# Kernel optimization log

Measured on AMD Instinct MI355X. Metric: run time of the kernel, lower is better.

Reference implementation:

```python
import jax, jax.numpy as jnp
import numpy as np

N = 16384
MUL0, MUL1, MUL2 = 128, 64, 32            # multiplicities of 0e, 1e, 2e
A = 16                                    # node_attr_dim (Ax0e)
D0, D1, D2 = MUL0, MUL1 * 3, MUL2 * 5     # e3nn flat block sizes
DIN = D0 + D1 + D2                        # 480
NGATE = MUL1 + MUL2                       # 96 gate scalars
OUT0 = MUL0 + NGATE                       # 224 scalar (0e) outputs of fctp_1


def setup_inputs() -> dict:
    key = jax.random.key(0)
    ks = jax.random.split(key, 10)
    f32 = jnp.float32
    return {
        "node_vec": jax.random.normal(ks[0], (N, DIN), f32),
        "node_embedding": jax.random.normal(ks[1], (N, A), f32),
        # fctp_1 path weights (fully-connected TP with Ax0e attr)
        "W1_l0": jax.random.normal(ks[2], (MUL0, A, OUT0), f32),
        "W1_l1": jax.random.normal(ks[3], (MUL1, A, MUL1), f32),
        "W1_l2": jax.random.normal(ks[4], (MUL2, A, MUL2), f32),
        "b1": jnp.zeros((OUT0,), f32),
        # fctp_2 scalar-path weight (only 0e x 0e -> 0e path exists)
        "W2": jax.random.normal(ks[5], (MUL0, A, A), f32),
        "b2": jnp.zeros((A,), f32),
        # scalar readout MLP: LinearRS -> SiLU -> LinearRS
        "W3": jax.random.normal(ks[6], (A, A), f32),
        "b3": jnp.zeros((A,), f32),
        "W4": jax.random.normal(ks[7], (A, 1), f32),
        "b4": jnp.zeros((1,), f32),
    }


def reference(node_vec, node_embedding, W1_l0, W1_l1, W1_l2, b1, W2, b2, W3, b3, W4, b4):
    # split e3nn-layout features into per-l blocks [N, mul, 2l+1]
    x0 = node_vec[:, :D0]                               # [N, 128]   l=0
    x1 = node_vec[:, D0:D0 + D1].reshape(-1, MUL1, 3)   # [N, 64, 3] l=1
    x2 = node_vec[:, D0 + D1:].reshape(-1, MUL2, 5)     # [N, 32, 5] l=2
    a = node_embedding                                  # [N, A] 0e scalars
    # fctp_1: fully-connected TP with Ax0e attr -> per-l bilinear mix (path-normalized)
    s = jnp.einsum('ni,na,iak->nk', x0, a, W1_l0) / np.sqrt(MUL0 * A) + b1  # [N, 224]
    y1 = jnp.einsum('nim,na,iak->nkm', x1, a, W1_l1) / np.sqrt(MUL1 * A)    # [N, 64, 3]
    y2 = jnp.einsum('nim,na,iak->nkm', x2, a, W1_l2) / np.sqrt(MUL2 * A)    # [N, 32, 5]
    # SwishGate: SiLU on scalars, sigmoid gates multiply the l>0 channels
    scalars = jax.nn.silu(s[:, :MUL0])
    gates = jax.nn.sigmoid(s[:, MUL0:])
    y1 = y1 * gates[:, :MUL1, None]
    y2 = y2 * gates[:, MUL1:, None]
    # fctp_2: output irreps = Ax0e, so only the 0e x 0e -> 0e path exists;
    # the gated l>0 features have no path to 0e (same as the torch TP).
    mid = jnp.einsum('ni,na,iak->nk', scalars, a, W2) / np.sqrt(MUL0 * A) + b2  # [N, A]
    # output_network: LinearRS -> SiLU -> LinearRS (rescale 1/sqrt(fan_in))
    h = jax.nn.silu(mid @ W3 / np.sqrt(A) + b3)
    return h @ W4 / np.sqrt(A) + b4                     # [N, 1]
```

## Files before the change

kernel.cpp:

```cpp
#include <hip/hip_runtime.h>


typedef _Float16 h8 __attribute__((ext_vector_type(8)));
typedef _Float16 h2 __attribute__((ext_vector_type(2)));
typedef float    f32x4 __attribute__((ext_vector_type(4)));
typedef unsigned int u32;

static __device__ __forceinline__ u32 pack2h(float a, float b) {
    h2 t = {(_Float16)a, (_Float16)b};
    return __builtin_bit_cast(u32, t);
}
static __device__ __forceinline__ f32x4 mfma_h(uint4 a, uint4 b, f32x4 c) {
    return __builtin_amdgcn_mfma_f32_16x16x32_f16(
        __builtin_bit_cast(h8, a), __builtin_bit_cast(h8, b), c, 0, 0, 0);
}
static __device__ __forceinline__ uint4 mk_afrag(_Float16 xh, const h2* ee) {
    h2 xx = {xh, xh};
    uint4 r;
    r.x = __builtin_bit_cast(u32, (h2)(xx * ee[0]));
    r.y = __builtin_bit_cast(u32, (h2)(xx * ee[1]));
    r.z = __builtin_bit_cast(u32, (h2)(xx * ee[2]));
    r.w = __builtin_bit_cast(u32, (h2)(xx * ee[3]));
    return r;
}

__global__ __launch_bounds__(256) void prep_kernel(
        const float* __restrict__ W1, const float* __restrict__ W2,
        _Float16* __restrict__ W1T, _Float16* __restrict__ W2T) {
    const int b = blockIdx.x, kc = b >> 2, tp = b & 3;
    const int tid = threadIdx.x;
    __shared__ float l1[32 * 36];
    __shared__ float l2[32 * 20];

    {
        int row = tid >> 3, c4 = tid & 7;
        float4 v = *(const float4*)(W1 + (size_t)(kc * 32 + row) * 224 + tp * 32 + c4 * 4);
        *(float4*)(l1 + row * 36 + c4 * 4) = v;
    }
    if (tp == 0 && tid < 128) {
        int row = tid >> 2, c4 = tid & 3;
        float4 v = *(const float4*)(W2 + (size_t)(kc * 32 + row) * 16 + c4 * 4);
        *(float4*)(l2 + row * 20 + c4 * 4) = v;
    }
    __syncthreads();

    if (tid < 128) {
        int tl = tid >> 6, t = tp * 2 + tl, lane = tid & 63;
        int q = lane >> 4, cc = lane & 15, colL = tl * 16 + cc;
        u32 w[4];
#pragma unroll
        for (int jj = 0; jj < 4; ++jj)
            w[jj] = pack2h(l1[(q * 8 + 2 * jj) * 36 + colL],
                           l1[(q * 8 + 2 * jj + 1) * 36 + colL]);
        *(uint4*)(W1T + (size_t)kc * 4096 + (t * 64 + lane) * 8) =
            make_uint4(w[0], w[1], w[2], w[3]);
    }
    if (tp == 0 && tid >= 128 && tid < 192) {
        int lane = tid - 128, q = lane >> 4, cc = lane & 15;
        u32 w[4];
#pragma unroll
        for (int jj = 0; jj < 4; ++jj)
            w[jj] = pack2h(l2[(q * 8 + 2 * jj) * 20 + cc],
                           l2[(q * 8 + 2 * jj + 1) * 20 + cc]);
        *(uint4*)(W2T + (size_t)kc * 512 + lane * 8) = make_uint4(w[0], w[1], w[2], w[3]);
    }
}

__global__ __launch_bounds__(1024, 4) void main_kernel(
        const float* __restrict__ node_vec, const float* __restrict__ emb,
        const _Float16* __restrict__ W1T, const _Float16* __restrict__ W2T,
        const float* __restrict__ b1, const float* __restrict__ b2,
        const float* __restrict__ W3, const float* __restrict__ b3,
        const float* __restrict__ W4, const float* __restrict__ b4,
        float* __restrict__ out) {
    __shared__ __align__(16) _Float16 xsh[2 * 4608 + 8];
    __shared__ __align__(16) char     uni[32768];
    __shared__ float w3s[256];
    __shared__ float b3s[16];
    __shared__ float w4s[16];
    __shared__ float b4s[1];

    _Float16* xe  = xsh;
    _Float16* xo  = xsh + 4608 + 8;
    float*    part = (float*)uni;
    float*    midp = (float*)uni;
    float*    mids = (float*)(uni + 17408);

    const int tid  = threadIdx.x;
    const int wave = tid >> 6, lane = tid & 63;
    const int q = lane >> 4, c = lane & 15;
    const int ih = q >> 1;
    const int aodd = q & 1;
    const int nodeBase = blockIdx.x * 64;

    for (int idx = tid; idx < 2048; idx += 1024) {
        int row = idx >> 5, c4 = idx & 31;
        float4 v = *(const float4*)(node_vec + (size_t)(nodeBase + row) * 480 + c4 * 4);
        h2 ev = {(_Float16)v.x, (_Float16)v.z};
        h2 ov = {(_Float16)v.y, (_Float16)v.w};
        *(h2*)(xe + row * 72 + c4 * 2) = ev;
        *(h2*)(xo + row * 72 + c4 * 2) = ov;
    }
    if (tid < 256) w3s[tid] = W3[tid];
    if (tid < 16) { b3s[tid] = b3[tid]; w4s[tid] = W4[tid]; }
    if (tid == 0) b4s[0] = b4[0];

    h2 eeg[4][4];
#pragma unroll
    for (int g = 0; g < 4; ++g) {
        const float* ep = emb + (size_t)(nodeBase + g * 16 + c) * 16 + aodd * 8;
        float4 v0 = *(const float4*)ep;
        float4 v1 = *(const float4*)(ep + 4);
        eeg[g][0] = (h2){(_Float16)v0.x, (_Float16)v0.y};
        eeg[g][1] = (h2){(_Float16)v0.z, (_Float16)v0.w};
        eeg[g][2] = (h2){(_Float16)v1.x, (_Float16)v1.y};
        eeg[g][3] = (h2){(_Float16)v1.z, (_Float16)v1.w};
    }
    __syncthreads();

    const int kh = wave >> 3;
    const int t  = wave & 7;
    f32x4 acc[4];
#pragma unroll
    for (int g = 0; g < 4; ++g) acc[g] = (f32x4){0.f, 0.f, 0.f, 0.f};

    const uint4* bp = (const uint4*)W1T + t * 64 + lane + kh * 32 * 512;
    const _Float16* xb = (ih ? xo : xe) + kh * 32;
    const _Float16* xr0 = xb + (0 * 16 + c) * 72;
    const _Float16* xr1 = xb + (1 * 16 + c) * 72;
    const _Float16* xr2 = xb + (2 * 16 + c) * 72;
    const _Float16* xr3 = xb + (3 * 16 + c) * 72;

    uint4 ring[8];
#pragma unroll
    for (int r = 0; r < 8; ++r) ring[r] = bp[r * 512];
    h8 xcur[4], xnxt[4];
    xcur[0] = *(const h8*)xr0;       xcur[1] = *(const h8*)xr1;
    xcur[2] = *(const h8*)xr2;       xcur[3] = *(const h8*)xr3;
    xnxt[0] = *(const h8*)(xr0 + 8); xnxt[1] = *(const h8*)(xr1 + 8);
    xnxt[2] = *(const h8*)(xr2 + 8); xnxt[3] = *(const h8*)(xr3 + 8);

#pragma unroll
    for (int bb = 0; bb < 4; ++bb) {
#pragma unroll
        for (int u = 0; u < 8; ++u) {
            const int kl = bb * 8 + u;
            uint4 cur = ring[u];
            ring[u] = bp[(kl + 8) * 512];
            acc[0] = mfma_h(mk_afrag(xcur[0][u], eeg[0]), cur, acc[0]);
            acc[1] = mfma_h(mk_afrag(xcur[1][u], eeg[1]), cur, acc[1]);
            acc[2] = mfma_h(mk_afrag(xcur[2][u], eeg[2]), cur, acc[2]);
            acc[3] = mfma_h(mk_afrag(xcur[3][u], eeg[3]), cur, acc[3]);
        }
        xcur[0] = xnxt[0]; xcur[1] = xnxt[1];
        xcur[2] = xnxt[2]; xcur[3] = xnxt[3];
        if (bb + 2 < 4) {
            const int o = (bb + 2) * 8;
            xnxt[0] = *(const h8*)(xr0 + o); xnxt[1] = *(const h8*)(xr1 + o);
            xnxt[2] = *(const h8*)(xr2 + o); xnxt[3] = *(const h8*)(xr3 + o);
        }
    }

    if (kh == 1) {
#pragma unroll
        for (int g = 0; g < 4; ++g)
            *(f32x4*)(part + (t * 16 + c) * 64 + g * 16 + q * 4) = acc[g];
    }
    __syncthreads();

    const float inv2048 = 0.022097086912079608f;
    if (kh == 0) {
        float bb1v = b1[t * 16 + c];
        _Float16* dst = (c & 1) ? xo : xe;
        int colh = t * 8 + (c >> 1);
#pragma unroll
        for (int g = 0; g < 4; ++g) {
            f32x4 p = *(const f32x4*)(part + (t * 16 + c) * 64 + g * 16 + q * 4);
#pragma unroll
            for (int r = 0; r < 4; ++r) {
                int node = g * 16 + q * 4 + r;
                float s  = (acc[g][r] + p[r]) * inv2048 + bb1v;
                float sc = s / (1.f + __expf(-s));
                dst[node * 72 + colh] = (_Float16)sc;
            }
        }
    }
    __syncthreads();

    {
        const int ng = wave >> 2, ks = wave & 3;
        const _Float16* srow = (ih ? xo : xe) + (ng * 16 + c) * 72 + ks * 16;
        h8 sa = *(const h8*)srow, sb = *(const h8*)(srow + 8);
        const uint4* b2p = (const uint4*)W2T + lane;
        f32x4 m0 = (f32x4){0.f, 0.f, 0.f, 0.f};
        uint4 wb[4];
#pragma unroll
        for (int u = 0; u < 4; ++u) wb[u] = b2p[(ks * 16 + u) * 64];
#pragma unroll
        for (int k2 = 0; k2 < 16; ++k2) {
            uint4 cur = wb[k2 & 3];
            if (k2 + 4 < 16) wb[k2 & 3] = b2p[(ks * 16 + k2 + 4) * 64];
            _Float16 sv = (k2 < 8) ? sa[k2] : sb[k2 - 8];
            m0 = mfma_h(mk_afrag(sv, eeg[ng]), cur, m0);
        }
#pragma unroll
        for (int r = 0; r < 4; ++r) {
            int node = ng * 16 + q * 4 + r;
            midp[(ks * 64 + node) * 17 + c] = m0[r];
        }
    }
    __syncthreads();

    {
        int node = tid >> 4, col = tid & 15;
        float m = midp[node * 17 + col] + midp[(64 + node) * 17 + col]
                + midp[(128 + node) * 17 + col] + midp[(192 + node) * 17 + col];
        mids[node * 17 + col] = m * inv2048 + b2[col];
    }
    __syncthreads();

    {
        int n = tid >> 4, jj = tid & 15;
        float a = 0.f;
#pragma unroll
        for (int cc = 0; cc < 16; ++cc) a += mids[n * 17 + cc] * w3s[cc * 16 + jj];
        a = a * 0.25f + b3s[jj];
        float hh = a / (1.f + __expf(-a));
        float po = hh * w4s[jj];
        po += __shfl_xor(po, 1);
        po += __shfl_xor(po, 2);
        po += __shfl_xor(po, 4);
        po += __shfl_xor(po, 8);
        if (jj == 0) out[nodeBase + n] = po * 0.25f + b4s[0];
    }
}

extern "C" void kernel_launch(void* const* d_in, const int* in_sizes, int n_in,
                              void* d_out, int out_size, void* d_ws, size_t ws_size,
                              hipStream_t stream) {
    const float* node_vec = (const float*)d_in[0];
    const float* emb      = (const float*)d_in[1];
    const float* W1       = (const float*)d_in[2];
    const float* b1v      = (const float*)d_in[5];
    const float* W2       = (const float*)d_in[6];
    const float* b2v      = (const float*)d_in[7];
    const float* W3       = (const float*)d_in[8];
    const float* b3v      = (const float*)d_in[9];
    const float* W4       = (const float*)d_in[10];
    const float* b4v      = (const float*)d_in[11];

    _Float16* W1T = (_Float16*)d_ws;
    _Float16* W2T = W1T + 64 * 4096;
    float* out = (float*)d_out;

    prep_kernel<<<256, 256, 0, stream>>>(W1, W2, W1T, W2T);
    main_kernel<<<256, 1024, 0, stream>>>(node_vec, emb, W1T, W2T,
                                          b1v, b2v, W3, b3v, W4, b4v, out);
}
```

Before: 113.3 us.

## Switch fctp_1 GEMM to 32x32x16 MFMA with 4-way K split

Replaces the 16x16x32 MFMA tiling of the first scalar tensor-product GEMM with 32x32x16 MFMA tiles, so each wave covers 32 output columns over two 32-node tiles and the K dimension is split four ways across wave groups instead of two. The weight prep kernel is rewritten to emit the matching fragment layout, and the node features are stored contiguously in fp16 instead of as even/odd split arrays. Partial sums are now reduced through LDS in fp16 over two extra barrier stages. The intent is fewer MFMA issues and more reuse of each weight fragment, at the cost of extra LDS traffic and syncs and some precision loss in the fp16 partials.

```diff
diff --git a/kernel.cpp b/kernel.cpp
--- a/kernel.cpp
+++ b/kernel.cpp
@@ -1,17 +1,22 @@
 #include <hip/hip_runtime.h>
 
 
-typedef _Float16 h8 __attribute__((ext_vector_type(8)));
-typedef _Float16 h2 __attribute__((ext_vector_type(2)));
-typedef float    f32x4 __attribute__((ext_vector_type(4)));
+typedef _Float16 h8  __attribute__((ext_vector_type(8)));
+typedef _Float16 h2  __attribute__((ext_vector_type(2)));
+typedef float    f32x4  __attribute__((ext_vector_type(4)));
+typedef float    f32x16 __attribute__((ext_vector_type(16)));
 typedef unsigned int u32;
 
 static __device__ __forceinline__ u32 pack2h(float a, float b) {
     h2 t = {(_Float16)a, (_Float16)b};
     return __builtin_bit_cast(u32, t);
 }
-static __device__ __forceinline__ f32x4 mfma_h(uint4 a, uint4 b, f32x4 c) {
+static __device__ __forceinline__ f32x4 mfma16(uint4 a, uint4 b, f32x4 c) {
     return __builtin_amdgcn_mfma_f32_16x16x32_f16(
+        __builtin_bit_cast(h8, a), __builtin_bit_cast(h8, b), c, 0, 0, 0);
+}
+static __device__ __forceinline__ f32x16 mfma32(uint4 a, uint4 b, f32x16 c) {
+    return __builtin_amdgcn_mfma_f32_32x32x16_f16(
         __builtin_bit_cast(h8, a), __builtin_bit_cast(h8, b), c, 0, 0, 0);
 }
 static __device__ __forceinline__ uint4 mk_afrag(_Float16 xh, const h2* ee) {
@@ -27,42 +32,43 @@
 __global__ __launch_bounds__(256) void prep_kernel(
         const float* __restrict__ W1, const float* __restrict__ W2,
         _Float16* __restrict__ W1T, _Float16* __restrict__ W2T) {
-    const int b = blockIdx.x, kc = b >> 2, tp = b & 3;
     const int tid = threadIdx.x;
-    __shared__ float l1[32 * 36];
-    __shared__ float l2[32 * 20];
-
-    {
-        int row = tid >> 3, c4 = tid & 7;
-        float4 v = *(const float4*)(W1 + (size_t)(kc * 32 + row) * 224 + tp * 32 + c4 * 4);
-        *(float4*)(l1 + row * 36 + c4 * 4) = v;
-    }
-    if (tp == 0 && tid < 128) {
-        int row = tid >> 2, c4 = tid & 3;
-        float4 v = *(const float4*)(W2 + (size_t)(kc * 32 + row) * 16 + c4 * 4);
-        *(float4*)(l2 + row * 20 + c4 * 4) = v;
-    }
-    __syncthreads();
-
-    if (tid < 128) {
-        int tl = tid >> 6, t = tp * 2 + tl, lane = tid & 63;
-        int q = lane >> 4, cc = lane & 15, colL = tl * 16 + cc;
+    if (blockIdx.x < 128) {
+        const int step = blockIdx.x;
+        __shared__ float l1[16 * 132];
+        for (int idx = tid; idx < 512; idx += 256) {
+            int row = idx >> 5, c4 = idx & 31;
+            float4 v = *(const float4*)(W1 + (size_t)(step * 16 + row) * 224 + c4 * 4);
+            *(float4*)(l1 + row * 132 + c4 * 4) = v;
+        }
+        __syncthreads();
+        const int t = tid >> 6, lane = tid & 63;
+        const int half = lane >> 5, col = t * 32 + (lane & 31);
         u32 w[4];
 #pragma unroll
         for (int jj = 0; jj < 4; ++jj)
-            w[jj] = pack2h(l1[(q * 8 + 2 * jj) * 36 + colL],
-                           l1[(q * 8 + 2 * jj + 1) * 36 + colL]);
-        *(uint4*)(W1T + (size_t)kc * 4096 + (t * 64 + lane) * 8) =
+            w[jj] = pack2h(l1[(half * 8 + 2 * jj) * 132 + col],
+                           l1[(half * 8 + 2 * jj + 1) * 132 + col]);
+        *(uint4*)(W1T + (size_t)((step * 4 + t) * 64 + lane) * 8) =
             make_uint4(w[0], w[1], w[2], w[3]);
-    }
-    if (tp == 0 && tid >= 128 && tid < 192) {
-        int lane = tid - 128, q = lane >> 4, cc = lane & 15;
-        u32 w[4];
-#pragma unroll
-        for (int jj = 0; jj < 4; ++jj)
-            w[jj] = pack2h(l2[(q * 8 + 2 * jj) * 20 + cc],
-                           l2[(q * 8 + 2 * jj + 1) * 20 + cc]);
-        *(uint4*)(W2T + (size_t)kc * 512 + lane * 8) = make_uint4(w[0], w[1], w[2], w[3]);
+    } else {
+        const int kc = blockIdx.x - 128;
+        __shared__ float l2[32 * 20];
+        if (tid < 128) {
+            int row = tid >> 2, c4 = tid & 3;
+            float4 v = *(const float4*)(W2 + (size_t)(kc * 32 + row) * 16 + c4 * 4);
+            *(float4*)(l2 + row * 20 + c4 * 4) = v;
+        }
+        __syncthreads();
+        if (tid < 64) {
+            int lane = tid, q = lane >> 4, cc = lane & 15;
+            u32 w[4];
+#pragma unroll
+            for (int jj = 0; jj < 4; ++jj)
+                w[jj] = pack2h(l2[(q * 8 + 2 * jj) * 20 + cc],
+                               l2[(q * 8 + 2 * jj + 1) * 20 + cc]);
+            *(uint4*)(W2T + (size_t)kc * 512 + lane * 8) = make_uint4(w[0], w[1], w[2], w[3]);
+        }
     }
 }
 
@@ -73,124 +79,142 @@
         const float* __restrict__ W3, const float* __restrict__ b3,
         const float* __restrict__ W4, const float* __restrict__ b4,
         float* __restrict__ out) {
-    __shared__ __align__(16) _Float16 xsh[2 * 4608 + 8];
-    __shared__ __align__(16) char     uni[32768];
+    __shared__ __align__(16) _Float16 xs[64 * 136];
+    __shared__ __align__(16) _Float16 sets[2 * 64 * 136];
     __shared__ float w3s[256];
     __shared__ float b3s[16];
     __shared__ float w4s[16];
     __shared__ float b4s[1];
 
-    _Float16* xe  = xsh;
-    _Float16* xo  = xsh + 4608 + 8;
-    float*    part = (float*)uni;
-    float*    midp = (float*)uni;
-    float*    mids = (float*)(uni + 17408);
+    _Float16* setA = sets;
+    _Float16* setB = sets + 64 * 136;
+    float*    midp = (float*)sets;
+    float*    mids = (float*)((char*)sets + 17408);
 
     const int tid  = threadIdx.x;
     const int wave = tid >> 6, lane = tid & 63;
-    const int q = lane >> 4, c = lane & 15;
-    const int ih = q >> 1;
-    const int aodd = q & 1;
+    const int l31 = lane & 31, half = lane >> 5;
     const int nodeBase = blockIdx.x * 64;
 
     for (int idx = tid; idx < 2048; idx += 1024) {
         int row = idx >> 5, c4 = idx & 31;
         float4 v = *(const float4*)(node_vec + (size_t)(nodeBase + row) * 480 + c4 * 4);
-        h2 ev = {(_Float16)v.x, (_Float16)v.z};
-        h2 ov = {(_Float16)v.y, (_Float16)v.w};
-        *(h2*)(xe + row * 72 + c4 * 2) = ev;
-        *(h2*)(xo + row * 72 + c4 * 2) = ov;
+        u32 p0 = pack2h(v.x, v.y), p1 = pack2h(v.z, v.w);
+        *(uint2*)(xs + row * 136 + c4 * 4) = make_uint2(p0, p1);
     }
     if (tid < 256) w3s[tid] = W3[tid];
     if (tid < 16) { b3s[tid] = b3[tid]; w4s[tid] = W4[tid]; }
     if (tid == 0) b4s[0] = b4[0];
 
-    h2 eeg[4][4];
-#pragma unroll
-    for (int g = 0; g < 4; ++g) {
-        const float* ep = emb + (size_t)(nodeBase + g * 16 + c) * 16 + aodd * 8;
+    h2 ee0[4], ee1[4];
+#pragma unroll
+    for (int mt = 0; mt < 2; ++mt) {
+        const float* ep = emb + (size_t)(nodeBase + mt * 32 + l31) * 16 + half * 8;
         float4 v0 = *(const float4*)ep;
         float4 v1 = *(const float4*)(ep + 4);
-        eeg[g][0] = (h2){(_Float16)v0.x, (_Float16)v0.y};
-        eeg[g][1] = (h2){(_Float16)v0.z, (_Float16)v0.w};
-        eeg[g][2] = (h2){(_Float16)v1.x, (_Float16)v1.y};
-        eeg[g][3] = (h2){(_Float16)v1.z, (_Float16)v1.w};
-    }
-    __syncthreads();
-
-    const int kh = wave >> 3;
-    const int t  = wave & 7;
-    f32x4 acc[4];
-#pragma unroll
-    for (int g = 0; g < 4; ++g) acc[g] = (f32x4){0.f, 0.f, 0.f, 0.f};
-
-    const uint4* bp = (const uint4*)W1T + t * 64 + lane + kh * 32 * 512;
-    const _Float16* xb = (ih ? xo : xe) + kh * 32;
-    const _Float16* xr0 = xb + (0 * 16 + c) * 72;
-    const _Float16* xr1 = xb + (1 * 16 + c) * 72;
-    const _Float16* xr2 = xb + (2 * 16 + c) * 72;
-    const _Float16* xr3 = xb + (3 * 16 + c) * 72;
+        h2* ee = mt ? ee1 : ee0;
+        ee[0] = (h2){(_Float16)v0.x, (_Float16)v0.y};
+        ee[1] = (h2){(_Float16)v0.z, (_Float16)v0.w};
+        ee[2] = (h2){(_Float16)v1.x, (_Float16)v1.y};
+        ee[3] = (h2){(_Float16)v1.z, (_Float16)v1.w};
+    }
+    __syncthreads();
+
+    const int kh = wave >> 2;
+    const int t  = wave & 3;
+    f32x16 acc0 = {0.f}, acc1 = {0.f};
+#pragma unroll
+    for (int r = 0; r < 16; ++r) { acc0[r] = 0.f; acc1[r] = 0.f; }
+
+    const uint4* bp = (const uint4*)W1T + ((kh * 32 * 4 + t) * 64 + lane);
+    const _Float16* xr0 = xs + (0 * 32 + l31) * 136 + kh * 32;
+    const _Float16* xr1 = xs + (1 * 32 + l31) * 136 + kh * 32;
 
     uint4 ring[8];
 #pragma unroll
-    for (int r = 0; r < 8; ++r) ring[r] = bp[r * 512];
-    h8 xcur[4], xnxt[4];
-    xcur[0] = *(const h8*)xr0;       xcur[1] = *(const h8*)xr1;
-    xcur[2] = *(const h8*)xr2;       xcur[3] = *(const h8*)xr3;
-    xnxt[0] = *(const h8*)(xr0 + 8); xnxt[1] = *(const h8*)(xr1 + 8);
-    xnxt[2] = *(const h8*)(xr2 + 8); xnxt[3] = *(const h8*)(xr3 + 8);
+    for (int r = 0; r < 8; ++r) ring[r] = bp[r * 256];
+    h8 xc0, xc1, xn0, xn1;
+    xc0 = *(const h8*)xr0;       xc1 = *(const h8*)xr1;
+    xn0 = *(const h8*)(xr0 + 8); xn1 = *(const h8*)(xr1 + 8);
 
 #pragma unroll
     for (int bb = 0; bb < 4; ++bb) {
 #pragma unroll
         for (int u = 0; u < 8; ++u) {
-            const int kl = bb * 8 + u;
             uint4 cur = ring[u];
-            ring[u] = bp[(kl + 8) * 512];
-            acc[0] = mfma_h(mk_afrag(xcur[0][u], eeg[0]), cur, acc[0]);
-            acc[1] = mfma_h(mk_afrag(xcur[1][u], eeg[1]), cur, acc[1]);
-            acc[2] = mfma_h(mk_afrag(xcur[2][u], eeg[2]), cur, acc[2]);
-            acc[3] = mfma_h(mk_afrag(xcur[3][u], eeg[3]), cur, acc[3]);
-        }
-        xcur[0] = xnxt[0]; xcur[1] = xnxt[1];
-        xcur[2] = xnxt[2]; xcur[3] = xnxt[3];
+            ring[u] = bp[(bb * 8 + u + 8) * 256];
+            acc0 = mfma32(mk_afrag(xc0[u], ee0), cur, acc0);
+            acc1 = mfma32(mk_afrag(xc1[u], ee1), cur, acc1);
+        }
+        xc0 = xn0; xc1 = xn1;
         if (bb + 2 < 4) {
-            const int o = (bb + 2) * 8;
-            xnxt[0] = *(const h8*)(xr0 + o); xnxt[1] = *(const h8*)(xr1 + o);
-            xnxt[2] = *(const h8*)(xr2 + o); xnxt[3] = *(const h8*)(xr3 + o);
-        }
-    }
-
+            xn0 = *(const h8*)(xr0 + (bb + 2) * 8);
+            xn1 = *(const h8*)(xr1 + (bb + 2) * 8);
+        }
+    }
+
+    const int colG = t * 32 + l31;
+#define ROWOF(r) (((r) & 3) + 8 * ((r) >> 2) + 4 * half)
+
+    if (kh >= 2) {
+        _Float16* st = (kh == 2) ? setA : setB;
+#pragma unroll
+        for (int r = 0; r < 16; ++r) {
+            int row = ROWOF(r);
+            st[(row)      * 136 + colG] = (_Float16)acc0[r];
+            st[(row + 32) * 136 + colG] = (_Float16)acc1[r];
+        }
+    }
+    __syncthreads();
+    if (kh < 2) {
+        const _Float16* st = (kh == 0) ? setA : setB;
+#pragma unroll
+        for (int r = 0; r < 16; ++r) {
+            int row = ROWOF(r);
+            acc0[r] += (float)st[(row)      * 136 + colG];
+            acc1[r] += (float)st[(row + 32) * 136 + colG];
+        }
+    }
+    __syncthreads();
     if (kh == 1) {
 #pragma unroll
-        for (int g = 0; g < 4; ++g)
-            *(f32x4*)(part + (t * 16 + c) * 64 + g * 16 + q * 4) = acc[g];
+        for (int r = 0; r < 16; ++r) {
+            int row = ROWOF(r);
+            setA[(row)      * 136 + colG] = (_Float16)acc0[r];
+            setA[(row + 32) * 136 + colG] = (_Float16)acc1[r];
+        }
     }
     __syncthreads();
 
     const float inv2048 = 0.022097086912079608f;
     if (kh == 0) {
-        float bb1v = b1[t * 16 + c];
-        _Float16* dst = (c & 1) ? xo : xe;
-        int colh = t * 8 + (c >> 1);
-#pragma unroll
-        for (int g = 0; g < 4; ++g) {
-            f32x4 p = *(const f32x4*)(part + (t * 16 + c) * 64 + g * 16 + q * 4);
-#pragma unroll
-            for (int r = 0; r < 4; ++r) {
-                int node = g * 16 + q * 4 + r;
-                float s  = (acc[g][r] + p[r]) * inv2048 + bb1v;
-                float sc = s / (1.f + __expf(-s));
-                dst[node * 72 + colh] = (_Float16)sc;
-            }
+        float bb1v = b1[colG];
+#pragma unroll
+        for (int r = 0; r < 16; ++r) {
+            int row = ROWOF(r);
+            float s0 = (acc0[r] + (float)setA[(row)      * 136 + colG]) * inv2048 + bb1v;
+            float s1 = (acc1[r] + (float)setA[(row + 32) * 136 + colG]) * inv2048 + bb1v;
+            xs[(row)      * 136 + colG] = (_Float16)(s0 / (1.f + __expf(-s0)));
+            xs[(row + 32) * 136 + colG] = (_Float16)(s1 / (1.f + __expf(-s1)));
         }
     }
     __syncthreads();
 
     {
         const int ng = wave >> 2, ks = wave & 3;
-        const _Float16* srow = (ih ? xo : xe) + (ng * 16 + c) * 72 + ks * 16;
-        h8 sa = *(const h8*)srow, sb = *(const h8*)(srow + 8);
+        const int q = lane >> 4, c = lane & 15;
+        const int ih = q >> 1, aodd = q & 1;
+        h2 ee[4];
+        {
+            const float* ep = emb + (size_t)(nodeBase + ng * 16 + c) * 16 + aodd * 8;
+            float4 v0 = *(const float4*)ep;
+            float4 v1 = *(const float4*)(ep + 4);
+            ee[0] = (h2){(_Float16)v0.x, (_Float16)v0.y};
+            ee[1] = (h2){(_Float16)v0.z, (_Float16)v0.w};
+            ee[2] = (h2){(_Float16)v1.x, (_Float16)v1.y};
+            ee[3] = (h2){(_Float16)v1.z, (_Float16)v1.w};
+        }
+        const _Float16* srow = xs + (ng * 16 + c) * 136;
         const uint4* b2p = (const uint4*)W2T + lane;
         f32x4 m0 = (f32x4){0.f, 0.f, 0.f, 0.f};
         uint4 wb[4];
@@ -200,8 +224,8 @@
         for (int k2 = 0; k2 < 16; ++k2) {
             uint4 cur = wb[k2 & 3];
             if (k2 + 4 < 16) wb[k2 & 3] = b2p[(ks * 16 + k2 + 4) * 64];
-            _Float16 sv = (k2 < 8) ? sa[k2] : sb[k2 - 8];
-            m0 = mfma_h(mk_afrag(sv, eeg[ng]), cur, m0);
+            _Float16 sv = srow[(ks * 16 + k2) * 2 + ih];
+            m0 = mfma16(mk_afrag(sv, ee), cur, m0);
         }
 #pragma unroll
         for (int r = 0; r < 4; ++r) {
@@ -233,6 +257,7 @@
         po += __shfl_xor(po, 8);
         if (jj == 0) out[nodeBase + n] = po * 0.25f + b4s[0];
     }
+#undef ROWOF
 }
 
 extern "C" void kernel_launch(void* const* d_in, const int* in_sizes, int n_in,
@@ -250,10 +275,10 @@
     const float* b4v      = (const float*)d_in[11];
 
     _Float16* W1T = (_Float16*)d_ws;
-    _Float16* W2T = W1T + 64 * 4096;
+    _Float16* W2T = W1T + 128 * 4 * 64 * 8;
     float* out = (float*)d_out;
 
-    prep_kernel<<<256, 256, 0, stream>>>(W1, W2, W1T, W2T);
+    prep_kernel<<<192, 256, 0, stream>>>(W1, W2, W1T, W2T);
     main_kernel<<<256, 1024, 0, stream>>>(node_vec, emb, W1T, W2T,
                                           b1v, b2v, W3, b3v, W4, b4v, out);
 }
```

After: 108.7 us. 1.04x faster.
